# Optimization experiments

Hardware: AMD Instinct MI355X
Metric: run time of the kernel (lower is better)

Reference implementation:

```python
import jax, jax.numpy as jnp
import numpy as np

BETA = 0.25
N, D, K = 131072, 128, 1024  # points, embed dim, codebook size


def setup_inputs() -> dict:
    key = jax.random.key(0)
    k1, k2 = jax.random.split(key)
    x = jax.random.normal(k1, (N, D), dtype=jnp.float32)
    emb = jax.random.normal(k2, (K, D), dtype=jnp.float32)  # codebook (nn.Embedding weight)
    return {"x": x, "emb": emb}


def reference(x, emb):
    dist = (jnp.sum(x * x, axis=1, keepdims=True)
            + jnp.sum(emb * emb, axis=1)
            - 2.0 * (x @ emb.T))
    index = jnp.argmin(dist, axis=1)          # [N]
    # one_hot @ emb == gather of nearest code
    quantized = emb[index]                    # [N, D]
    commitment_loss = jnp.mean((jax.lax.stop_gradient(quantized) - x) ** 2)
    embedding_loss = jnp.mean((quantized - jax.lax.stop_gradient(x)) ** 2)
    vq_loss = commitment_loss * BETA + embedding_loss
    # straight-through estimator
    quantized_st = x + jax.lax.stop_gradient(quantized - x)
    return index[:, None], quantized_st, vq_loss
```

## Files before the change

### kernel.cpp

```cpp
#include <hip/hip_runtime.h>

#define NPTS 131072
#define DIM  128
#define KC   1024
#define CHB  16640

using half8 = __attribute__((ext_vector_type(8))) _Float16;
using f32x4 = __attribute__((ext_vector_type(4))) float;

static __device__ __forceinline__ unsigned umax_(unsigned a, unsigned b){ return a > b ? a : b; }
static __device__ __forceinline__ unsigned med3u(unsigned a, unsigned b, unsigned c){
    unsigned d;
    asm("v_med3_u32 %0, %1, %2, %3" : "=v"(d) : "v"(a), "v"(b), "v"(c));
    return d;
}


__global__ void vq_prep(const float* __restrict__ emb, unsigned short* __restrict__ wsE,
                        float* __restrict__ eeW) {
    int lane = threadIdx.x & 63, wv = threadIdx.x >> 6;
    int code = blockIdx.x * 4 + wv;
    const float* e = emb + (size_t)code * DIM;
    float a = e[lane], b = e[lane + 64];

    int chunk = code >> 6, r = code & 63;
    int ct = r >> 4, c = r & 15;
    int kc = lane >> 5, g = (lane >> 3) & 3, j = lane & 7;
    size_t off = (size_t)chunk * 16384 + (size_t)(ct * 4096 + kc * 1024 + g * 256 + c * 16 + j * 2);
    _Float16 ha = (_Float16)a, hb = (_Float16)b;
    wsE[off >> 1]          = __builtin_bit_cast(unsigned short, ha);
    wsE[(off + 2048) >> 1] = __builtin_bit_cast(unsigned short, hb);

    float v = a * a + b * b;
    #pragma unroll
    for (int o = 32; o > 0; o >>= 1) v += __shfl_down(v, o);
    if (lane == 0) eeW[code] = 0.5f * v - 512.0f;
}

__global__ __launch_bounds__(256, 1) void vq_mfma(const float* __restrict__ x,
                                                  const float* __restrict__ emb,
                                                  const unsigned short* __restrict__ wsE,
                                                  const float* __restrict__ eeW,
                                                  float* __restrict__ out,
                                                  float* __restrict__ bsum) {
    __shared__ __attribute__((aligned(128))) char lds[2][CHB];
    const int tid  = threadIdx.x;
    const int lane = tid & 63, wv = tid >> 6;
    const int g    = lane >> 4, c = lane & 15;
    const int blockbase = blockIdx.x * 128;

    half8 ah[2][4];
    #pragma unroll
    for (int rt = 0; rt < 2; ++rt) {
        const float* xr = x + (size_t)(blockbase + wv * 32 + rt * 16 + c) * DIM;
        #pragma unroll
        for (int kc = 0; kc < 4; ++kc) {
            const float4* p = reinterpret_cast<const float4*>(xr + kc * 32 + g * 8);
            float4 v0 = p[0], v1 = p[1];
            half8 hh;
            hh[0] = (_Float16)v0.x; hh[1] = (_Float16)v0.y;
            hh[2] = (_Float16)v0.z; hh[3] = (_Float16)v0.w;
            hh[4] = (_Float16)v1.x; hh[5] = (_Float16)v1.y;
            hh[6] = (_Float16)v1.z; hh[7] = (_Float16)v1.w;
            ah[rt][kc] = hh;
        }
    }

    unsigned m1[8], m2[8], m3[8];
    #pragma unroll
    for (int i = 0; i < 8; ++i) { m1[i] = 0u; m2[i] = 0u; m3[i] = 0u; }

    #define STAGE(BUF, CH)                                                                   \
        do {                                                                                 \
            const char* src_ = (const char*)wsE + (size_t)(CH) * 16384 + (size_t)wv * 4096;  \
            char* dst_ = &lds[(BUF)][0] + wv * 4096;                                         \
            _Pragma("unroll")                                                                \
            for (int it = 0; it < 4; ++it) {                                                 \
                __builtin_amdgcn_global_load_lds(                                            \
                    (const __attribute__((address_space(1))) void*)(src_ + it * 1024 + lane * 16), \
                    (__attribute__((address_space(3))) void*)(dst_ + it * 1024),             \
                    16, 0, 0);                                                               \
            }                                                                                \
            if (wv == 0) {                                                                   \
                __builtin_amdgcn_global_load_lds(                                            \
                    (const __attribute__((address_space(1))) void*)(eeW + (size_t)(CH) * 64 + lane), \
                    (__attribute__((address_space(3))) void*)(&lds[(BUF)][0] + 16384),       \
                    4, 0, 0);                                                                \
            }                                                                                \
        } while (0)

    STAGE(0, 0);
    __syncthreads();

    for (int ch = 0; ch < 16; ++ch) {
        if (ch < 15) STAGE((ch + 1) & 1, ch + 1);
        const char* L  = &lds[ch & 1][0];
        const char* Lf = L + (size_t)(lane << 4);

        #pragma unroll
        for (int ct = 0; ct < 4; ++ct) {
            const float eec = *reinterpret_cast<const float*>(L + 16384 + ((ct * 16 + c) << 2));
            f32x4 acc0 = {-eec, -eec, -eec, -eec};
            f32x4 acc1 = {-eec, -eec, -eec, -eec};
            half8 b0 = *reinterpret_cast<const half8*>(Lf + (ct * 4096 + 0 * 1024));
            half8 b1 = *reinterpret_cast<const half8*>(Lf + (ct * 4096 + 1 * 1024));
            half8 b2 = *reinterpret_cast<const half8*>(Lf + (ct * 4096 + 2 * 1024));
            half8 b3 = *reinterpret_cast<const half8*>(Lf + (ct * 4096 + 3 * 1024));
            acc0 = __builtin_amdgcn_mfma_f32_16x16x32_f16(ah[0][0], b0, acc0, 0, 0, 0);
            acc1 = __builtin_amdgcn_mfma_f32_16x16x32_f16(ah[1][0], b0, acc1, 0, 0, 0);
            acc0 = __builtin_amdgcn_mfma_f32_16x16x32_f16(ah[0][1], b1, acc0, 0, 0, 0);
            acc1 = __builtin_amdgcn_mfma_f32_16x16x32_f16(ah[1][1], b1, acc1, 0, 0, 0);
            acc0 = __builtin_amdgcn_mfma_f32_16x16x32_f16(ah[0][2], b2, acc0, 0, 0, 0);
            acc1 = __builtin_amdgcn_mfma_f32_16x16x32_f16(ah[1][2], b2, acc1, 0, 0, 0);
            acc0 = __builtin_amdgcn_mfma_f32_16x16x32_f16(ah[0][3], b3, acc0, 0, 0, 0);
            acc1 = __builtin_amdgcn_mfma_f32_16x16x32_f16(ah[1][3], b3, acc1, 0, 0, 0);

            const unsigned codeC = (unsigned)(1023 - (ch * 64 + ct * 16 + c));
            #pragma unroll
            for (int q = 0; q < 4; ++q) {
                #pragma unroll
                for (int rt = 0; rt < 2; ++rt) {
                    float sp = (rt ? acc1[q] : acc0[q]);
                    unsigned u   = __builtin_bit_cast(unsigned, sp);
                    unsigned key = (u & 0xFFFFFC00u) | codeC;
                    const int i = rt * 4 + q;
                    m3[i] = med3u(m2[i], m3[i], key);
                    m2[i] = med3u(m1[i], m2[i], key);
                    m1[i] = umax_(m1[i], key);
                }
            }
        }
        __syncthreads();
    }

    int* lbest = reinterpret_cast<int*>(&lds[0][0]);
    #pragma unroll
    for (int rt = 0; rt < 2; ++rt) {
        #pragma unroll
        for (int q = 0; q < 4; ++q) {
            const int i = rt * 4 + q;
            unsigned a1 = m1[i], a2 = m2[i], a3 = m3[i];
            #pragma unroll
            for (int mk = 1; mk < 16; mk <<= 1) {
                unsigned b1 = (unsigned)__shfl_xor((int)a1, mk, 64);
                unsigned b2 = (unsigned)__shfl_xor((int)a2, mk, 64);
                unsigned b3 = (unsigned)__shfl_xor((int)a3, mk, 64);
                unsigned c1 = umax_(a1, b1), t1 = (a1 < b1 ? a1 : b1);
                unsigned u1 = umax_(a2, b2), u2 = (a2 < b2 ? a2 : b2);
                unsigned c2 = umax_(t1, u1), t2 = (t1 < u1 ? t1 : u1);
                unsigned c3 = umax_(umax_(t2, u2), umax_(a3, b3));
                a1 = c1; a2 = c2; a3 = c3;
            }
            if (c == 0) {
                int lr = wv * 32 + rt * 16 + g * 4 + q;
                int i1 = 1023 - (int)(a1 & 1023u);
                int i2 = 1023 - (int)(a2 & 1023u);
                int i3 = 1023 - (int)(a3 & 1023u);
                lbest[lr] = i1 | (i2 << 10) | (i3 << 20);
            }
        }
    }
    __syncthreads();

    {
        const int lrow = tid >> 1, hf = tid & 1;
        const int grow = blockbase + lrow;
        const int pk = lbest[lrow];
        const int ia = pk & 1023, ib = (pk >> 10) & 1023, ic = (pk >> 20) & 1023;

        const float4* xv4 = reinterpret_cast<const float4*>(x + (size_t)grow * DIM + hf * 64);
        const float4* ea = reinterpret_cast<const float4*>(emb + (size_t)ia * DIM + hf * 64);
        const float4* eb = reinterpret_cast<const float4*>(emb + (size_t)ib * DIM + hf * 64);
        const float4* ec = reinterpret_cast<const float4*>(emb + (size_t)ic * DIM + hf * 64);
        float da = 0.f, db = 0.f, dc = 0.f;
        #pragma unroll 4
        for (int i = 0; i < 16; ++i) {
            float4 xx = xv4[i];
            float4 va = ea[i], vb = eb[i], vc = ec[i];
            float ax = va.x - xx.x, ay = va.y - xx.y, az = va.z - xx.z, aw = va.w - xx.w;
            float bx = vb.x - xx.x, by = vb.y - xx.y, bz = vb.z - xx.z, bw = vb.w - xx.w;
            float cx = vc.x - xx.x, cy = vc.y - xx.y, cz = vc.z - xx.z, cw = vc.w - xx.w;
            da += ax * ax + ay * ay + az * az + aw * aw;
            db += bx * bx + by * by + bz * bz + bw * bw;
            dc += cx * cx + cy * cy + cz * cz + cw * cw;
        }
        da += __shfl_xor(da, 1, 64);
        db += __shfl_xor(db, 1, 64);
        dc += __shfl_xor(dc, 1, 64);

        int idx = ia; float dm = da;
        if (db < dm || (db == dm && ib < idx)) { dm = db; idx = ib; }
        if (dc < dm || (dc == dm && ic < idx)) { dm = dc; idx = ic; }

        if (hf == 0) out[grow] = (float)idx;

        const float4* q4 = reinterpret_cast<const float4*>(emb + (size_t)idx * DIM + hf * 64);
        float4* oq = reinterpret_cast<float4*>(out + (size_t)NPTS + (size_t)grow * DIM + hf * 64);
        #pragma unroll
        for (int i = 0; i < 16; ++i) oq[i] = q4[i];

        float lsum = (hf == 0) ? dm : 0.f;
        __shared__ float red[4];
        #pragma unroll
        for (int o = 32; o > 0; o >>= 1) lsum += __shfl_down(lsum, o);
        if (lane == 0) red[wv] = lsum;
        __syncthreads();
        if (tid == 0) bsum[blockIdx.x] = (red[0] + red[1]) + (red[2] + red[3]);
    }
    #undef STAGE
}

__global__ void vq_finalize(const float* __restrict__ bsum, float* __restrict__ out) {
    __shared__ float red[16];
    int t = threadIdx.x;
    float v = bsum[t];
    #pragma unroll
    for (int o = 32; o > 0; o >>= 1) v += __shfl_down(v, o);
    if ((t & 63) == 0) red[t >> 6] = v;
    __syncthreads();
    if (t == 0) {
        float s = 0.f;
        #pragma unroll
        for (int i = 0; i < 16; ++i) s += red[i];
        out[(size_t)NPTS + (size_t)NPTS * DIM] = 1.25f * s / 16777216.0f;
    }
}

__global__ void vq_ee(const float* __restrict__ emb, float* __restrict__ eeW) {
    int gid  = blockIdx.x * blockDim.x + threadIdx.x;
    int w    = gid >> 6;
    int lane = threadIdx.x & 63;
    const float* e = emb + (size_t)w * DIM;
    float a = e[lane];
    float b = e[lane + 64];
    float v = a * a + b * b;
    #pragma unroll
    for (int o = 32; o > 0; o >>= 1) v += __shfl_down(v, o);
    if (lane == 0) eeW[w] = 0.5f * v - 512.0f;
}

__global__ __launch_bounds__(256, 1) void vq_main(const float* __restrict__ x,
                                                  const float* __restrict__ emb,
                                                  const float* __restrict__ eeW,
                                                  float* __restrict__ out,
                                                  float* __restrict__ bsum) {
    const int p = blockIdx.x * 256 + threadIdx.x;
    float4 xr[32];
    const float4* xv = reinterpret_cast<const float4*>(x + (size_t)p * DIM);
    #pragma unroll
    for (int i = 0; i < 32; ++i) xr[i] = xv[i];
    float bestv = -3.4e38f; int bi = 0;
    for (int k = 0; k < KC; ++k) {
        const int ku = __builtin_amdgcn_readfirstlane(k);
        const float4* e4 = reinterpret_cast<const float4*>(emb + (size_t)ku * DIM);
        float a0 = 0.f, a1 = 0.f, a2 = 0.f, a3 = 0.f;
        #pragma unroll
        for (int i = 0; i < 32; ++i) {
            float4 ev = e4[i];
            a0 = fmaf(xr[i].x, ev.x, a0);
            a1 = fmaf(xr[i].y, ev.y, a1);
            a2 = fmaf(xr[i].z, ev.z, a2);
            a3 = fmaf(xr[i].w, ev.w, a3);
        }
        float s = ((a0 + a1) + (a2 + a3)) - eeW[ku];
        if (s > bestv) { bestv = s; bi = k; }
    }
    out[p] = (float)bi;
    const float4* q4 = reinterpret_cast<const float4*>(emb + (size_t)bi * DIM);
    float4* oq = reinterpret_cast<float4*>(out + (size_t)NPTS + (size_t)p * DIM);
    float lsum = 0.f;
    #pragma unroll
    for (int i = 0; i < 32; ++i) {
        float4 qv = q4[i];
        oq[i] = qv;
        float dx = qv.x - xr[i].x;
        float dy = qv.y - xr[i].y;
        float dz = qv.z - xr[i].z;
        float dw = qv.w - xr[i].w;
        lsum += dx * dx + dy * dy + dz * dz + dw * dw;
    }
    __shared__ float red[4];
    #pragma unroll
    for (int o = 32; o > 0; o >>= 1) lsum += __shfl_down(lsum, o);
    int lane = threadIdx.x & 63, wvl = threadIdx.x >> 6;
    if (lane == 0) red[wvl] = lsum;
    __syncthreads();
    if (threadIdx.x == 0) bsum[blockIdx.x] = (red[0] + red[1]) + (red[2] + red[3]);
}

__global__ void vq_finalize512(const float* __restrict__ bsum, float* __restrict__ out) {
    __shared__ float red[8];
    int t = threadIdx.x;
    float v = bsum[t];
    #pragma unroll
    for (int o = 32; o > 0; o >>= 1) v += __shfl_down(v, o);
    if ((t & 63) == 0) red[t >> 6] = v;
    __syncthreads();
    if (t == 0) {
        float s = 0.f;
        #pragma unroll
        for (int i = 0; i < 8; ++i) s += red[i];
        out[(size_t)NPTS + (size_t)NPTS * DIM] = 1.25f * s / 16777216.0f;
    }
}

extern "C" void kernel_launch(void* const* d_in, const int* in_sizes, int n_in,
                              void* d_out, int out_size, void* d_ws, size_t ws_size,
                              hipStream_t stream) {
    const float* x   = (const float*)d_in[0];
    const float* emb = (const float*)d_in[1];
    float* out = (float*)d_out;
    char*  ws  = (char*)d_ws;

    if (ws_size >= 270336) {
        unsigned short* wsE = (unsigned short*)ws;
        float* eeW  = (float*)(ws + 262144);
        float* bsum = (float*)(ws + 266240);
        vq_prep<<<256, 256, 0, stream>>>(emb, wsE, eeW);
        vq_mfma<<<1024, 256, 0, stream>>>(x, emb, wsE, eeW, out, bsum);
        vq_finalize<<<1, 1024, 0, stream>>>(bsum, out);
    } else {
        float* eeW  = (float*)ws;
        float* bsum = (float*)ws + 1024;
        vq_ee<<<256, 256, 0, stream>>>(emb, eeW);
        vq_main<<<512, 256, 0, stream>>>(x, emb, eeW, out, bsum);
        vq_finalize512<<<1, 512, 0, stream>>>(bsum, out);
    }
}
```

Baseline: 124.2 us.

## Load codebook fragments straight from global/L2 instead of LDS double buffering

Removes the LDS double-buffered staging of the fp16 codebook and eeW chunks along with the per-chunk block barriers. Each wave now reads its MFMA B fragments and bias values directly from global memory, relying on L1/L2 caching of the small shared codebook. Launch bounds are raised to two blocks per CU so that more occupancy can hide the extra global-load latency. The cost is more cache traffic and exposed load latency, since there is no explicit prefetch and the loop is marked not to unroll.

```diff
diff --git a/kernel.cpp b/kernel.cpp
--- a/kernel.cpp
+++ b/kernel.cpp
@@ -3,7 +3,6 @@
 #define NPTS 131072
 #define DIM  128
 #define KC   1024
-#define CHB  16640
 
 using half8 = __attribute__((ext_vector_type(8))) _Float16;
 using f32x4 = __attribute__((ext_vector_type(4))) float;
@@ -37,13 +36,14 @@
     if (lane == 0) eeW[code] = 0.5f * v - 512.0f;
 }
 
-__global__ __launch_bounds__(256, 1) void vq_mfma(const float* __restrict__ x,
+__global__ __launch_bounds__(256, 2) void vq_mfma(const float* __restrict__ x,
                                                   const float* __restrict__ emb,
                                                   const unsigned short* __restrict__ wsE,
                                                   const float* __restrict__ eeW,
                                                   float* __restrict__ out,
                                                   float* __restrict__ bsum) {
-    __shared__ __attribute__((aligned(128))) char lds[2][CHB];
+    __shared__ int   lbest[128];
+    __shared__ float red[4];
     const int tid  = threadIdx.x;
     const int lane = tid & 63, wv = tid >> 6;
     const int g    = lane >> 4, c = lane & 15;
@@ -70,42 +70,21 @@
     #pragma unroll
     for (int i = 0; i < 8; ++i) { m1[i] = 0u; m2[i] = 0u; m3[i] = 0u; }
 
-    #define STAGE(BUF, CH)                                                                   \
-        do {                                                                                 \
-            const char* src_ = (const char*)wsE + (size_t)(CH) * 16384 + (size_t)wv * 4096;  \
-            char* dst_ = &lds[(BUF)][0] + wv * 4096;                                         \
-            _Pragma("unroll")                                                                \
-            for (int it = 0; it < 4; ++it) {                                                 \
-                __builtin_amdgcn_global_load_lds(                                            \
-                    (const __attribute__((address_space(1))) void*)(src_ + it * 1024 + lane * 16), \
-                    (__attribute__((address_space(3))) void*)(dst_ + it * 1024),             \
-                    16, 0, 0);                                                               \
-            }                                                                                \
-            if (wv == 0) {                                                                   \
-                __builtin_amdgcn_global_load_lds(                                            \
-                    (const __attribute__((address_space(1))) void*)(eeW + (size_t)(CH) * 64 + lane), \
-                    (__attribute__((address_space(3))) void*)(&lds[(BUF)][0] + 16384),       \
-                    4, 0, 0);                                                                \
-            }                                                                                \
-        } while (0)
-
-    STAGE(0, 0);
-    __syncthreads();
-
+    const char* Wl = (const char*)wsE + (size_t)(lane << 4);
+
+    #pragma unroll 1
     for (int ch = 0; ch < 16; ++ch) {
-        if (ch < 15) STAGE((ch + 1) & 1, ch + 1);
-        const char* L  = &lds[ch & 1][0];
-        const char* Lf = L + (size_t)(lane << 4);
-
+        const char* Cb = Wl + (size_t)ch * 16384;
         #pragma unroll
         for (int ct = 0; ct < 4; ++ct) {
-            const float eec = *reinterpret_cast<const float*>(L + 16384 + ((ct * 16 + c) << 2));
+            half8 b0 = *reinterpret_cast<const half8*>(Cb + (ct * 4096 + 0 * 1024));
+            half8 b1 = *reinterpret_cast<const half8*>(Cb + (ct * 4096 + 1 * 1024));
+            half8 b2 = *reinterpret_cast<const half8*>(Cb + (ct * 4096 + 2 * 1024));
+            half8 b3 = *reinterpret_cast<const half8*>(Cb + (ct * 4096 + 3 * 1024));
+            const float eec = eeW[ch * 64 + ct * 16 + c];
+
             f32x4 acc0 = {-eec, -eec, -eec, -eec};
             f32x4 acc1 = {-eec, -eec, -eec, -eec};
-            half8 b0 = *reinterpret_cast<const half8*>(Lf + (ct * 4096 + 0 * 1024));
-            half8 b1 = *reinterpret_cast<const half8*>(Lf + (ct * 4096 + 1 * 1024));
-            half8 b2 = *reinterpret_cast<const half8*>(Lf + (ct * 4096 + 2 * 1024));
-            half8 b3 = *reinterpret_cast<const half8*>(Lf + (ct * 4096 + 3 * 1024));
             acc0 = __builtin_amdgcn_mfma_f32_16x16x32_f16(ah[0][0], b0, acc0, 0, 0, 0);
             acc1 = __builtin_amdgcn_mfma_f32_16x16x32_f16(ah[1][0], b0, acc1, 0, 0, 0);
             acc0 = __builtin_amdgcn_mfma_f32_16x16x32_f16(ah[0][1], b1, acc0, 0, 0, 0);
@@ -130,10 +109,8 @@
                 }
             }
         }
-        __syncthreads();
-    }
-
-    int* lbest = reinterpret_cast<int*>(&lds[0][0]);
+    }
+
     #pragma unroll
     for (int rt = 0; rt < 2; ++rt) {
         #pragma unroll
@@ -200,14 +177,12 @@
         for (int i = 0; i < 16; ++i) oq[i] = q4[i];
 
         float lsum = (hf == 0) ? dm : 0.f;
-        __shared__ float red[4];
         #pragma unroll
         for (int o = 32; o > 0; o >>= 1) lsum += __shfl_down(lsum, o);
         if (lane == 0) red[wv] = lsum;
         __syncthreads();
         if (tid == 0) bsum[blockIdx.x] = (red[0] + red[1]) + (red[2] + red[3]);
     }
-    #undef STAGE
 }
 
 __global__ void vq_finalize(const float* __restrict__ bsum, float* __restrict__ out) {
```

Result: slower. 154.8 us (+24.7%).

## Split each block's 128 rows across 8 waves of 16 rows instead of 4 waves

Applied to the files above, without the earlier changes.

The MFMA kernel now launches 512 threads per block, and each wave owns 16 rows instead of 32. Every wave loads half as much of each codebook chunk into LDS, issues half the MFMAs per chunk, and keeps half the top-3 registers. The refinement epilogue now uses 4 threads per row instead of 2. The aim is more waves per CU to hide the latency of LDS loads, MFMA and global memory, at the cost of each B-fragment LDS read being reused across only one row tile instead of two.

```diff
diff --git a/kernel.cpp b/kernel.cpp
--- a/kernel.cpp
+++ b/kernel.cpp
@@ -3,7 +3,6 @@
 #define NPTS 131072
 #define DIM  128
 #define KC   1024
-#define CHB  16640
 
 using half8 = __attribute__((ext_vector_type(8))) _Float16;
 using f32x4 = __attribute__((ext_vector_type(4))) float;
@@ -37,22 +36,23 @@
     if (lane == 0) eeW[code] = 0.5f * v - 512.0f;
 }
 
-__global__ __launch_bounds__(256, 1) void vq_mfma(const float* __restrict__ x,
+__global__ __launch_bounds__(512, 1) void vq_mfma(const float* __restrict__ x,
                                                   const float* __restrict__ emb,
                                                   const unsigned short* __restrict__ wsE,
                                                   const float* __restrict__ eeW,
                                                   float* __restrict__ out,
                                                   float* __restrict__ bsum) {
-    __shared__ __attribute__((aligned(128))) char lds[2][CHB];
+    __shared__ __attribute__((aligned(128))) char lds[2][16640];
+    __shared__ int   lbest[128];
+    __shared__ float red[8];
     const int tid  = threadIdx.x;
     const int lane = tid & 63, wv = tid >> 6;
     const int g    = lane >> 4, c = lane & 15;
     const int blockbase = blockIdx.x * 128;
 
-    half8 ah[2][4];
-    #pragma unroll
-    for (int rt = 0; rt < 2; ++rt) {
-        const float* xr = x + (size_t)(blockbase + wv * 32 + rt * 16 + c) * DIM;
+    half8 ah[4];
+    {
+        const float* xr = x + (size_t)(blockbase + wv * 16 + c) * DIM;
         #pragma unroll
         for (int kc = 0; kc < 4; ++kc) {
             const float4* p = reinterpret_cast<const float4*>(xr + kc * 32 + g * 8);
@@ -62,20 +62,20 @@
             hh[2] = (_Float16)v0.z; hh[3] = (_Float16)v0.w;
             hh[4] = (_Float16)v1.x; hh[5] = (_Float16)v1.y;
             hh[6] = (_Float16)v1.z; hh[7] = (_Float16)v1.w;
-            ah[rt][kc] = hh;
-        }
-    }
-
-    unsigned m1[8], m2[8], m3[8];
-    #pragma unroll
-    for (int i = 0; i < 8; ++i) { m1[i] = 0u; m2[i] = 0u; m3[i] = 0u; }
+            ah[kc] = hh;
+        }
+    }
+
+    unsigned m1[4], m2[4], m3[4];
+    #pragma unroll
+    for (int i = 0; i < 4; ++i) { m1[i] = 0u; m2[i] = 0u; m3[i] = 0u; }
 
     #define STAGE(BUF, CH)                                                                   \
         do {                                                                                 \
-            const char* src_ = (const char*)wsE + (size_t)(CH) * 16384 + (size_t)wv * 4096;  \
-            char* dst_ = &lds[(BUF)][0] + wv * 4096;                                         \
+            const char* src_ = (const char*)wsE + (size_t)(CH) * 16384 + (size_t)wv * 2048;  \
+            char* dst_ = &lds[(BUF)][0] + wv * 2048;                                         \
             _Pragma("unroll")                                                                \
-            for (int it = 0; it < 4; ++it) {                                                 \
+            for (int it = 0; it < 2; ++it) {                                                 \
                 __builtin_amdgcn_global_load_lds(                                            \
                     (const __attribute__((address_space(1))) void*)(src_ + it * 1024 + lane * 16), \
                     (__attribute__((address_space(3))) void*)(dst_ + it * 1024),             \
@@ -100,81 +100,67 @@
         #pragma unroll
         for (int ct = 0; ct < 4; ++ct) {
             const float eec = *reinterpret_cast<const float*>(L + 16384 + ((ct * 16 + c) << 2));
-            f32x4 acc0 = {-eec, -eec, -eec, -eec};
-            f32x4 acc1 = {-eec, -eec, -eec, -eec};
             half8 b0 = *reinterpret_cast<const half8*>(Lf + (ct * 4096 + 0 * 1024));
             half8 b1 = *reinterpret_cast<const half8*>(Lf + (ct * 4096 + 1 * 1024));
             half8 b2 = *reinterpret_cast<const half8*>(Lf + (ct * 4096 + 2 * 1024));
             half8 b3 = *reinterpret_cast<const half8*>(Lf + (ct * 4096 + 3 * 1024));
-            acc0 = __builtin_amdgcn_mfma_f32_16x16x32_f16(ah[0][0], b0, acc0, 0, 0, 0);
-            acc1 = __builtin_amdgcn_mfma_f32_16x16x32_f16(ah[1][0], b0, acc1, 0, 0, 0);
-            acc0 = __builtin_amdgcn_mfma_f32_16x16x32_f16(ah[0][1], b1, acc0, 0, 0, 0);
-            acc1 = __builtin_amdgcn_mfma_f32_16x16x32_f16(ah[1][1], b1, acc1, 0, 0, 0);
-            acc0 = __builtin_amdgcn_mfma_f32_16x16x32_f16(ah[0][2], b2, acc0, 0, 0, 0);
-            acc1 = __builtin_amdgcn_mfma_f32_16x16x32_f16(ah[1][2], b2, acc1, 0, 0, 0);
-            acc0 = __builtin_amdgcn_mfma_f32_16x16x32_f16(ah[0][3], b3, acc0, 0, 0, 0);
-            acc1 = __builtin_amdgcn_mfma_f32_16x16x32_f16(ah[1][3], b3, acc1, 0, 0, 0);
+            f32x4 acc = {-eec, -eec, -eec, -eec};
+            acc = __builtin_amdgcn_mfma_f32_16x16x32_f16(ah[0], b0, acc, 0, 0, 0);
+            acc = __builtin_amdgcn_mfma_f32_16x16x32_f16(ah[1], b1, acc, 0, 0, 0);
+            acc = __builtin_amdgcn_mfma_f32_16x16x32_f16(ah[2], b2, acc, 0, 0, 0);
+            acc = __builtin_amdgcn_mfma_f32_16x16x32_f16(ah[3], b3, acc, 0, 0, 0);
 
             const unsigned codeC = (unsigned)(1023 - (ch * 64 + ct * 16 + c));
             #pragma unroll
             for (int q = 0; q < 4; ++q) {
-                #pragma unroll
-                for (int rt = 0; rt < 2; ++rt) {
-                    float sp = (rt ? acc1[q] : acc0[q]);
-                    unsigned u   = __builtin_bit_cast(unsigned, sp);
-                    unsigned key = (u & 0xFFFFFC00u) | codeC;
-                    const int i = rt * 4 + q;
-                    m3[i] = med3u(m2[i], m3[i], key);
-                    m2[i] = med3u(m1[i], m2[i], key);
-                    m1[i] = umax_(m1[i], key);
-                }
+                float sp = acc[q];
+                unsigned u   = __builtin_bit_cast(unsigned, sp);
+                unsigned key = (u & 0xFFFFFC00u) | codeC;
+                m3[q] = med3u(m2[q], m3[q], key);
+                m2[q] = med3u(m1[q], m2[q], key);
+                m1[q] = umax_(m1[q], key);
             }
         }
         __syncthreads();
     }
 
-    int* lbest = reinterpret_cast<int*>(&lds[0][0]);
-    #pragma unroll
-    for (int rt = 0; rt < 2; ++rt) {
-        #pragma unroll
-        for (int q = 0; q < 4; ++q) {
-            const int i = rt * 4 + q;
-            unsigned a1 = m1[i], a2 = m2[i], a3 = m3[i];
-            #pragma unroll
-            for (int mk = 1; mk < 16; mk <<= 1) {
-                unsigned b1 = (unsigned)__shfl_xor((int)a1, mk, 64);
-                unsigned b2 = (unsigned)__shfl_xor((int)a2, mk, 64);
-                unsigned b3 = (unsigned)__shfl_xor((int)a3, mk, 64);
-                unsigned c1 = umax_(a1, b1), t1 = (a1 < b1 ? a1 : b1);
-                unsigned u1 = umax_(a2, b2), u2 = (a2 < b2 ? a2 : b2);
-                unsigned c2 = umax_(t1, u1), t2 = (t1 < u1 ? t1 : u1);
-                unsigned c3 = umax_(umax_(t2, u2), umax_(a3, b3));
-                a1 = c1; a2 = c2; a3 = c3;
-            }
-            if (c == 0) {
-                int lr = wv * 32 + rt * 16 + g * 4 + q;
-                int i1 = 1023 - (int)(a1 & 1023u);
-                int i2 = 1023 - (int)(a2 & 1023u);
-                int i3 = 1023 - (int)(a3 & 1023u);
-                lbest[lr] = i1 | (i2 << 10) | (i3 << 20);
-            }
+    #pragma unroll
+    for (int q = 0; q < 4; ++q) {
+        unsigned a1 = m1[q], a2 = m2[q], a3 = m3[q];
+        #pragma unroll
+        for (int mk = 1; mk < 16; mk <<= 1) {
+            unsigned b1 = (unsigned)__shfl_xor((int)a1, mk, 64);
+            unsigned b2 = (unsigned)__shfl_xor((int)a2, mk, 64);
+            unsigned b3 = (unsigned)__shfl_xor((int)a3, mk, 64);
+            unsigned c1 = umax_(a1, b1), t1 = (a1 < b1 ? a1 : b1);
+            unsigned u1 = umax_(a2, b2), u2 = (a2 < b2 ? a2 : b2);
+            unsigned c2 = umax_(t1, u1), t2 = (t1 < u1 ? t1 : u1);
+            unsigned c3 = umax_(umax_(t2, u2), umax_(a3, b3));
+            a1 = c1; a2 = c2; a3 = c3;
+        }
+        if (c == 0) {
+            int lr = wv * 16 + g * 4 + q;
+            int i1 = 1023 - (int)(a1 & 1023u);
+            int i2 = 1023 - (int)(a2 & 1023u);
+            int i3 = 1023 - (int)(a3 & 1023u);
+            lbest[lr] = i1 | (i2 << 10) | (i3 << 20);
         }
     }
     __syncthreads();
 
     {
-        const int lrow = tid >> 1, hf = tid & 1;
+        const int lrow = tid >> 2, qd = tid & 3;
         const int grow = blockbase + lrow;
         const int pk = lbest[lrow];
         const int ia = pk & 1023, ib = (pk >> 10) & 1023, ic = (pk >> 20) & 1023;
 
-        const float4* xv4 = reinterpret_cast<const float4*>(x + (size_t)grow * DIM + hf * 64);
-        const float4* ea = reinterpret_cast<const float4*>(emb + (size_t)ia * DIM + hf * 64);
-        const float4* eb = reinterpret_cast<const float4*>(emb + (size_t)ib * DIM + hf * 64);
-        const float4* ec = reinterpret_cast<const float4*>(emb + (size_t)ic * DIM + hf * 64);
+        const float4* xv4 = reinterpret_cast<const float4*>(x + (size_t)grow * DIM + qd * 32);
+        const float4* ea = reinterpret_cast<const float4*>(emb + (size_t)ia * DIM + qd * 32);
+        const float4* eb = reinterpret_cast<const float4*>(emb + (size_t)ib * DIM + qd * 32);
+        const float4* ec = reinterpret_cast<const float4*>(emb + (size_t)ic * DIM + qd * 32);
         float da = 0.f, db = 0.f, dc = 0.f;
         #pragma unroll 4
-        for (int i = 0; i < 16; ++i) {
+        for (int i = 0; i < 8; ++i) {
             float4 xx = xv4[i];
             float4 va = ea[i], vb = eb[i], vc = ec[i];
             float ax = va.x - xx.x, ay = va.y - xx.y, az = va.z - xx.z, aw = va.w - xx.w;
@@ -184,28 +170,32 @@
             db += bx * bx + by * by + bz * bz + bw * bw;
             dc += cx * cx + cy * cy + cz * cz + cw * cw;
         }
-        da += __shfl_xor(da, 1, 64);
-        db += __shfl_xor(db, 1, 64);
-        dc += __shfl_xor(dc, 1, 64);
+        da += __shfl_xor(da, 1, 64); da += __shfl_xor(da, 2, 64);
+        db += __shfl_xor(db, 1, 64); db += __shfl_xor(db, 2, 64);
+        dc += __shfl_xor(dc, 1, 64); dc += __shfl_xor(dc, 2, 64);
 
         int idx = ia; float dm = da;
         if (db < dm || (db == dm && ib < idx)) { dm = db; idx = ib; }
         if (dc < dm || (dc == dm && ic < idx)) { dm = dc; idx = ic; }
 
-        if (hf == 0) out[grow] = (float)idx;
-
-        const float4* q4 = reinterpret_cast<const float4*>(emb + (size_t)idx * DIM + hf * 64);
-        float4* oq = reinterpret_cast<float4*>(out + (size_t)NPTS + (size_t)grow * DIM + hf * 64);
-        #pragma unroll
-        for (int i = 0; i < 16; ++i) oq[i] = q4[i];
-
-        float lsum = (hf == 0) ? dm : 0.f;
-        __shared__ float red[4];
+        if (qd == 0) out[grow] = (float)idx;
+
+        const float4* q4 = reinterpret_cast<const float4*>(emb + (size_t)idx * DIM + qd * 32);
+        float4* oq = reinterpret_cast<float4*>(out + (size_t)NPTS + (size_t)grow * DIM + qd * 32);
+        #pragma unroll
+        for (int i = 0; i < 8; ++i) oq[i] = q4[i];
+
+        float lsum = (qd == 0) ? dm : 0.f;
         #pragma unroll
         for (int o = 32; o > 0; o >>= 1) lsum += __shfl_down(lsum, o);
         if (lane == 0) red[wv] = lsum;
         __syncthreads();
-        if (tid == 0) bsum[blockIdx.x] = (red[0] + red[1]) + (red[2] + red[3]);
+        if (tid == 0) {
+            float s = 0.f;
+            #pragma unroll
+            for (int i = 0; i < 8; ++i) s += red[i];
+            bsum[blockIdx.x] = s;
+        }
     }
     #undef STAGE
 }
@@ -317,7 +307,7 @@
         float* eeW  = (float*)(ws + 262144);
         float* bsum = (float*)(ws + 266240);
         vq_prep<<<256, 256, 0, stream>>>(emb, wsE, eeW);
-        vq_mfma<<<1024, 256, 0, stream>>>(x, emb, wsE, eeW, out, bsum);
+        vq_mfma<<<1024, 512, 0, stream>>>(x, emb, wsE, eeW, out, bsum);
         vq_finalize<<<1, 1024, 0, stream>>>(bsum, out);
     } else {
         float* eeW  = (float*)ws;
```

New measurement: 120.9 us. 1.03x faster.
